# Optimization experiments

Measured on AMD Instinct MI355X. Metric: run time of the kernel, lower is better.

## Reference

```python
import jax, jax.numpy as jnp
import numpy as np

N_TOKENS = 32768
LATENT_DIM = 512
N_EMBED = 8192
BETA_COMMIT = 0.25


def setup_inputs() -> dict:
    key = jax.random.key(0)
    k_x, k_w, _ = jax.random.split(key, 3)
    x = jax.random.normal(k_x, (N_TOKENS, LATENT_DIM), dtype=jnp.float32)
    # nn.init.uniform_ -> U[0, 1)
    W = jax.random.uniform(k_w, (N_EMBED, LATENT_DIM), dtype=jnp.float32)
    temperature = jnp.ones((1,), dtype=jnp.float32)
    return {"x": x, "temperature": temperature, "W": W}


def reference(x, temperature, W):
    # out_proj is Identity (sim_vq=False, codebook_normalization=False)
    codebook = W  # [K, D]
    # Squared-Euclidean pairwise distances: [N, K]
    dist = (
        jnp.sum(x * x, axis=1, keepdims=True)
        + jnp.sum(codebook * codebook, axis=1)[None, :]
        - 2.0 * (x @ codebook.T)
    )
    ids = jnp.argmin(dist, axis=1)  # [N]
    emb = codebook[ids]             # gather nearest code, [N, D]
    # Straight-through estimator (training STE path)
    emb_out = x + jax.lax.stop_gradient(emb - x)
    # QuantizeLoss(beta): codebook loss + beta * commitment loss
    codebook_loss = jnp.mean(jnp.sum((jax.lax.stop_gradient(x) - emb) ** 2, axis=-1))
    commit_loss = jnp.mean(jnp.sum((x - jax.lax.stop_gradient(emb)) ** 2, axis=-1))
    loss = codebook_loss + BETA_COMMIT * commit_loss
    return emb_out, ids, loss
```

## Files before the change

kernel.cpp:

```cpp
#include <hip/hip_runtime.h>
#include <math.h>

#define NTOK 32768
#define DIM 512
#define KC 8192

#define BM 256
#define BN 256
#define HSTEPS 16
#define VSTEPS 48
#define NBUF 4
#define STEP_U16 8192

typedef unsigned short u16;
typedef _Float16 half8 __attribute__((ext_vector_type(8)));
typedef float f32x4 __attribute__((ext_vector_type(4)));

__device__ __forceinline__ void gload16(const void* g, void* l) {
    __builtin_amdgcn_global_load_lds(
        (const __attribute__((address_space(1))) unsigned int*)(void*)g,
        (__attribute__((address_space(3))) unsigned int*)l, 16, 0, 0);
}

__global__ __launch_bounds__(256) void c2_kernel(const float* __restrict__ W,
                                                 float* __restrict__ c2) {
    int wid = threadIdx.x >> 6;
    int lane = threadIdx.x & 63;
    int row = blockIdx.x * 4 + wid;
    const float* wr = W + (size_t)row * DIM;
    float s = 0.f;
#pragma unroll
    for (int q = 0; q < 2; ++q) {
        float4 v = *(const float4*)(wr + q * 256 + lane * 4);
        s += v.x * v.x + v.y * v.y + v.z * v.z + v.w * v.w;
    }
#pragma unroll
    for (int off = 32; off > 0; off >>= 1) s += __shfl_down(s, off);
    if (lane == 0) c2[row] = s;
}

__global__ __launch_bounds__(256) void loss_kernel(const float* __restrict__ partials,
                                                   float* __restrict__ lossp) {
    __shared__ float red[256];
    float s = 0.f;
    for (int idx = threadIdx.x; idx < NTOK / 4; idx += 256) s += partials[idx];
    red[threadIdx.x] = s;
    __syncthreads();
    for (int off = 128; off > 0; off >>= 1) {
        if (threadIdx.x < off) red[threadIdx.x] += red[threadIdx.x + off];
        __syncthreads();
    }
    if (threadIdx.x == 0) lossp[0] = 1.25f * red[0] / (float)NTOK;
}

__global__ void init_keys_kernel(unsigned long long* keys) {
    keys[blockIdx.x * 256 + threadIdx.x] = ~0ull;
}

__global__ __launch_bounds__(256) void split_kernel(const float* __restrict__ src,
                                                    u16* __restrict__ dst) {
    int lane = threadIdx.x & 63;
    int wid = threadIdx.x >> 6;
    int row = blockIdx.x * 64 + lane;
    int s = blockIdx.y * 4 + wid;
    const float* p = src + (size_t)row * DIM + s * 32;
    int tile = row >> 8, Rl = row & 255, swz = (Rl >> 1) & 3;
    u16* baseH = dst + ((size_t)(tile * 32 + s) * 256 + Rl) * 32;
    u16* baseL = baseH + (size_t)HSTEPS * STEP_U16;
#pragma unroll
    for (int c = 0; c < 4; ++c) {
        float4 va = ((const float4*)p)[c * 2];
        float4 vb = ((const float4*)p)[c * 2 + 1];
        float f[8] = {va.x, va.y, va.z, va.w, vb.x, vb.y, vb.z, vb.w};
        unsigned H[4], L[4];
#pragma unroll
        for (int j = 0; j < 4; ++j) {
            _Float16 h0 = (_Float16)f[2 * j];
            _Float16 g0 = (_Float16)(f[2 * j] - (float)h0);
            _Float16 h1 = (_Float16)f[2 * j + 1];
            _Float16 g1 = (_Float16)(f[2 * j + 1] - (float)h1);
            H[j] = (unsigned)__builtin_bit_cast(u16, h0) |
                   ((unsigned)__builtin_bit_cast(u16, h1) << 16);
            L[j] = (unsigned)__builtin_bit_cast(u16, g0) |
                   ((unsigned)__builtin_bit_cast(u16, g1) << 16);
        }
        int slot = (c ^ swz) * 8;
        *(uint4*)(baseH + slot) = uint4{H[0], H[1], H[2], H[3]};
        *(uint4*)(baseL + slot) = uint4{L[0], L[1], L[2], L[3]};
    }
}

__global__ __launch_bounds__(512, 2) void argmin_mfma_kernel(
    const u16* __restrict__ xscr, const u16* __restrict__ wscr,
    const float* __restrict__ c2, unsigned long long* __restrict__ keys) {
    __shared__ __align__(16) u16 Ab[NBUF][STEP_U16];
    __shared__ __align__(16) u16 Bb[NBUF][STEP_U16];

    int cpx = (int)gridDim.x >> 3;
    int bid = (int)blockIdx.x;
    int wg = (bid & 7) * cpx + (bid >> 3);
    int tcol = wg & 31;
    int trow = wg >> 5;

    const int tid = threadIdx.x;
    const int lane = tid & 63;
    const int w = tid >> 6;
    const int wr = w >> 2;
    const int wc = w & 3;

    const u16* gA = xscr + (size_t)trow * (32 * STEP_U16);
    const u16* gB = wscr + (size_t)tcol * (32 * STEP_U16);

    const int l15 = lane & 15, q = lane >> 4;
    float c2v[4];
    const int colbase = tcol * 256 + wc * 64 + l15;
#pragma unroll
    for (int n = 0; n < 4; ++n) c2v[n] = c2[colbase + n * 16];

    f32x4 acc[8][4];
#pragma unroll
    for (int m = 0; m < 8; ++m)
#pragma unroll
        for (int n = 0; n < 4; ++n) acc[m][n] = f32x4{0.f, 0.f, 0.f, 0.f};

    const int swz = (l15 >> 1) & 3;
    const int aoff0 = (wr * 128 + l15) * 32 + (q ^ swz) * 8;
    const int boff0 = (wc * 64 + l15) * 32 + (q ^ swz) * 8;
    const int wo = w * 512;
    const int lo8 = lane * 8;

#pragma unroll
    for (int p = 0; p < 3; ++p) {
        const u16* ga = gA + (size_t)p * STEP_U16;
        const u16* gb = gB + (size_t)p * STEP_U16;
#pragma unroll
        for (int r = 0; r < 2; ++r) {
            gload16(ga + r * 4096 + wo + lo8, Ab[p] + r * 4096 + wo);
            gload16(gb + r * 4096 + wo + lo8, Bb[p] + r * 4096 + wo);
        }
    }
    asm volatile("s_waitcnt vmcnt(8)" ::: "memory");
    __builtin_amdgcn_s_barrier();
    __builtin_amdgcn_sched_barrier(0);

#pragma unroll 4
    for (int v = 0; v < VSTEPS; ++v) {
        if (v + 3 < VSTEPS) {
            int u = v + 3;
            int sa = (u < 32) ? u : u - 32;
            int sb = (u < 16) ? u : u - 16;
            const u16* ga = gA + (size_t)sa * STEP_U16;
            const u16* gb = gB + (size_t)sb * STEP_U16;
            u16* la = Ab[u & 3];
            u16* lb = Bb[u & 3];
#pragma unroll
            for (int r = 0; r < 2; ++r) {
                gload16(ga + r * 4096 + wo + lo8, la + r * 4096 + wo);
                gload16(gb + r * 4096 + wo + lo8, lb + r * 4096 + wo);
            }
        }
        const u16* A = Ab[v & 3];
        const u16* B = Bb[v & 3];
        half8 b[4], a[8];
#pragma unroll
        for (int n = 0; n < 4; ++n) b[n] = *(const half8*)(B + boff0 + n * 512);
#pragma unroll
        for (int m = 0; m < 8; ++m) a[m] = *(const half8*)(A + aoff0 + m * 512);
        __builtin_amdgcn_s_setprio(1);
#pragma unroll
        for (int m = 0; m < 8; ++m)
#pragma unroll
            for (int n = 0; n < 4; ++n)
                acc[m][n] = __builtin_amdgcn_mfma_f32_16x16x32_f16(a[m], b[n], acc[m][n], 0, 0, 0);
        __builtin_amdgcn_s_setprio(0);
        asm volatile("s_waitcnt vmcnt(8)" ::: "memory");
        __builtin_amdgcn_s_barrier();
        __builtin_amdgcn_sched_barrier(0);
    }

    unsigned long long* kbuf = (unsigned long long*)&Ab[0][0];
#pragma unroll
    for (int m = 0; m < 8; ++m) {
#pragma unroll
        for (int r = 0; r < 4; ++r) {
            float bv = 3.4e38f;
            int bi = 0;
#pragma unroll
            for (int n = 0; n < 4; ++n) {
                float sc = c2v[n] - 2.0f * acc[m][n][r];
                int idx = colbase + n * 16;
                if (sc < bv) { bv = sc; bi = idx; }
            }
#pragma unroll
            for (int off = 1; off < 16; off <<= 1) {
                float ov = __shfl_xor(bv, off);
                int oi = __shfl_xor(bi, off);
                if (ov < bv || (ov == bv && oi < bi)) { bv = ov; bi = oi; }
            }
            if (l15 == 0) {
                unsigned u = __float_as_uint(bv);
                u = (u & 0x80000000u) ? ~u : (u | 0x80000000u);
                kbuf[wc * 256 + wr * 128 + m * 16 + q * 4 + r] =
                    ((unsigned long long)u << 32) | (unsigned)bi;
            }
        }
    }
    __syncthreads();
    if (tid < 256) {
        unsigned long long k = kbuf[tid];
#pragma unroll
        for (int c = 1; c < 4; ++c) {
            unsigned long long o = kbuf[c * 256 + tid];
            if (o < k) k = o;
        }
        atomicMin(&keys[trow * 256 + tid], k);
    }
}

__global__ __launch_bounds__(256) void gather_keys_kernel(
    const float* __restrict__ x, const float* __restrict__ W,
    const unsigned long long* __restrict__ keys, float* __restrict__ emb_out,
    float* __restrict__ idsf, float* __restrict__ partials) {
    int wid = threadIdx.x >> 6;
    int lane = threadIdx.x & 63;
    int tok = blockIdx.x * 4 + wid;
    int id = (int)(unsigned)(keys[tok] & 0xffffffffull);
    if (lane == 0) idsf[tok] = (float)id;
    const float* wr = W + (size_t)id * DIM;
    const float* xr = x + (size_t)tok * DIM;
    float* orow = emb_out + (size_t)tok * DIM;
    float s = 0.f;
#pragma unroll
    for (int q = 0; q < 2; ++q) {
        int d = q * 256 + lane * 4;
        float4 wv = *(const float4*)(wr + d);
        float4 xv = *(const float4*)(xr + d);
        float4 e = {xv.x + (wv.x - xv.x), xv.y + (wv.y - xv.y),
                    xv.z + (wv.z - xv.z), xv.w + (wv.w - xv.w)};
        *(float4*)(orow + d) = e;
        float dx = xv.x - wv.x, dy = xv.y - wv.y, dz = xv.z - wv.z, dw = xv.w - wv.w;
        s += dx * dx + dy * dy + dz * dz + dw * dw;
    }
#pragma unroll
    for (int off = 32; off > 0; off >>= 1) s += __shfl_down(s, off);
    __shared__ float bsum[4];
    if (lane == 0) bsum[wid] = s;
    __syncthreads();
    if (threadIdx.x == 0)
        partials[blockIdx.x] = bsum[0] + bsum[1] + bsum[2] + bsum[3];
}

#define FBN 64
#define FBK 64
#define FDC 32
#define FPAD 68
__global__ __launch_bounds__(256) void argmin_kernel(const float* __restrict__ x,
                                                     const float* __restrict__ W,
                                                     const float* __restrict__ c2,
                                                     float* __restrict__ idsf) {
    __shared__ float xs[FDC][FPAD];
    __shared__ float wt[FDC][FPAD];
    __shared__ float c2s[FBK];
    __shared__ float redv[16][FBN];
    __shared__ int redi[16][FBN];
    const int tid = threadIdx.x;
    const int n0 = blockIdx.x * FBN;
    const int i = tid & 15;
    const int j = tid >> 4;
    float bestv[4];
    int besti[4];
#pragma unroll
    for (int t = 0; t < 4; ++t) { bestv[t] = 3.4e38f; besti[t] = 0; }
    for (int k0 = 0; k0 < KC; k0 += FBK) {
        __syncthreads();
        if (tid < FBK) c2s[tid] = c2[k0 + tid];
        float acc[4][4];
#pragma unroll
        for (int a = 0; a < 4; ++a)
#pragma unroll
            for (int b = 0; b < 4; ++b) acc[a][b] = 0.f;
        for (int d0 = 0; d0 < DIM; d0 += FDC) {
            __syncthreads();
#pragma unroll
            for (int r = 0; r < 2; ++r) {
                int f = tid + r * 256;
                int tok = f >> 3;
                int dq = f & 7;
                float4 xv = *(const float4*)(x + (size_t)(n0 + tok) * DIM + d0 + dq * 4);
                float4 wv = *(const float4*)(W + (size_t)(k0 + tok) * DIM + d0 + dq * 4);
                xs[dq * 4 + 0][tok] = xv.x; xs[dq * 4 + 1][tok] = xv.y;
                xs[dq * 4 + 2][tok] = xv.z; xs[dq * 4 + 3][tok] = xv.w;
                wt[dq * 4 + 0][tok] = wv.x; wt[dq * 4 + 1][tok] = wv.y;
                wt[dq * 4 + 2][tok] = wv.z; wt[dq * 4 + 3][tok] = wv.w;
            }
            __syncthreads();
#pragma unroll
            for (int d = 0; d < FDC; ++d) {
                float4 xv = *(const float4*)(&xs[d][i * 4]);
                float4 wv = *(const float4*)(&wt[d][j * 4]);
#pragma unroll
                for (int a = 0; a < 4; ++a) {
                    float xa = (a == 0) ? xv.x : (a == 1) ? xv.y : (a == 2) ? xv.z : xv.w;
                    acc[a][0] = fmaf(xa, wv.x, acc[a][0]);
                    acc[a][1] = fmaf(xa, wv.y, acc[a][1]);
                    acc[a][2] = fmaf(xa, wv.z, acc[a][2]);
                    acc[a][3] = fmaf(xa, wv.w, acc[a][3]);
                }
            }
        }
#pragma unroll
        for (int ti = 0; ti < 4; ++ti)
#pragma unroll
            for (int cj = 0; cj < 4; ++cj) {
                float s = c2s[j * 4 + cj] - 2.f * acc[ti][cj];
                int kk = k0 + j * 4 + cj;
                if (s < bestv[ti]) { bestv[ti] = s; besti[ti] = kk; }
            }
    }
#pragma unroll
    for (int ti = 0; ti < 4; ++ti) {
        redv[j][i * 4 + ti] = bestv[ti];
        redi[j][i * 4 + ti] = besti[ti];
    }
    __syncthreads();
    if (tid < FBN) {
        float bv = redv[0][tid];
        int bi = redi[0][tid];
#pragma unroll
        for (int jj = 1; jj < 16; ++jj) {
            float v = redv[jj][tid];
            int ii = redi[jj][tid];
            if (v < bv || (v == bv && ii < bi)) { bv = v; bi = ii; }
        }
        idsf[n0 + tid] = (float)bi;
    }
}

__global__ __launch_bounds__(256) void gather_kernel(const float* __restrict__ x,
                                                     const float* __restrict__ W,
                                                     const float* __restrict__ idsf,
                                                     float* __restrict__ emb_out,
                                                     float* __restrict__ partials) {
    int wid = threadIdx.x >> 6;
    int lane = threadIdx.x & 63;
    int tok = blockIdx.x * 4 + wid;
    int id = (int)idsf[tok];
    const float* wr = W + (size_t)id * DIM;
    const float* xr = x + (size_t)tok * DIM;
    float* orow = emb_out + (size_t)tok * DIM;
    float s = 0.f;
#pragma unroll
    for (int q = 0; q < 2; ++q) {
        int d = q * 256 + lane * 4;
        float4 wv = *(const float4*)(wr + d);
        float4 xv = *(const float4*)(xr + d);
        float4 e = {xv.x + (wv.x - xv.x), xv.y + (wv.y - xv.y),
                    xv.z + (wv.z - xv.z), xv.w + (wv.w - xv.w)};
        *(float4*)(orow + d) = e;
        float dx = xv.x - wv.x, dy = xv.y - wv.y, dz = xv.z - wv.z, dw = xv.w - wv.w;
        s += dx * dx + dy * dy + dz * dz + dw * dw;
    }
#pragma unroll
    for (int off = 32; off > 0; off >>= 1) s += __shfl_down(s, off);
    __shared__ float bsum[4];
    if (lane == 0) bsum[wid] = s;
    __syncthreads();
    if (threadIdx.x == 0)
        partials[blockIdx.x] = bsum[0] + bsum[1] + bsum[2] + bsum[3];
}

extern "C" void kernel_launch(void* const* d_in, const int* in_sizes, int n_in,
                              void* d_out, int out_size, void* d_ws, size_t ws_size,
                              hipStream_t stream) {
    const float* x = (const float*)d_in[0];
    const float* W = (const float*)d_in[2];

    float* out = (float*)d_out;
    float* emb_out = out;
    float* idsf = out + (size_t)NTOK * DIM;
    float* lossp = idsf + NTOK;

    const size_t W12_BYTES = (size_t)KC * DIM * 4;
    const size_t KEYS_BYTES = (size_t)NTOK * 8;
    size_t need = W12_BYTES + KEYS_BYTES + (size_t)KC * 4 + (size_t)(NTOK / 4) * 4;

    if (ws_size >= need) {
        u16* w12 = (u16*)d_ws;
        unsigned long long* keys = (unsigned long long*)((char*)d_ws + W12_BYTES);
        float* c2 = (float*)((char*)keys + KEYS_BYTES);
        float* partials = c2 + KC;
        u16* x12 = (u16*)emb_out;

        split_kernel<<<dim3(NTOK / 64, 4), 256, 0, stream>>>(x, x12);
        split_kernel<<<dim3(KC / 64, 4), 256, 0, stream>>>(W, w12);
        c2_kernel<<<KC / 4, 256, 0, stream>>>(W, c2);
        init_keys_kernel<<<NTOK / 256, 256, 0, stream>>>(keys);
        argmin_mfma_kernel<<<(NTOK / BM) * (KC / BN), 512, 0, stream>>>(x12, w12, c2, keys);
        gather_keys_kernel<<<NTOK / 4, 256, 0, stream>>>(x, W, keys, emb_out, idsf, partials);
        loss_kernel<<<1, 256, 0, stream>>>(partials, lossp);
    } else {
        float* c2 = (float*)d_ws;
        float* partials = c2 + KC;
        c2_kernel<<<KC / 4, 256, 0, stream>>>(W, c2);
        argmin_kernel<<<NTOK / FBN, 256, 0, stream>>>(x, W, c2, idsf);
        gather_kernel<<<NTOK / 4, 256, 0, stream>>>(x, W, idsf, emb_out, partials);
        loss_kernel<<<1, 256, 0, stream>>>(partials, lossp);
    }
}
```

Before: 958.7 us.

## Split GEMM main loop into two half-phases interleaving LDS reads, prefetch and MFMA

```diff
diff --git a/kernel.cpp b/kernel.cpp
--- a/kernel.cpp
+++ b/kernel.cpp
@@ -133,11 +133,10 @@
     for (int p = 0; p < 3; ++p) {
         const u16* ga = gA + (size_t)p * STEP_U16;
         const u16* gb = gB + (size_t)p * STEP_U16;
-#pragma unroll
-        for (int r = 0; r < 2; ++r) {
-            gload16(ga + r * 4096 + wo + lo8, Ab[p] + r * 4096 + wo);
-            gload16(gb + r * 4096 + wo + lo8, Bb[p] + r * 4096 + wo);
-        }
+        gload16(ga + wo + lo8, Ab[p] + wo);
+        gload16(ga + 4096 + wo + lo8, Ab[p] + 4096 + wo);
+        gload16(gb + wo + lo8, Bb[p] + wo);
+        gload16(gb + 4096 + wo + lo8, Bb[p] + 4096 + wo);
     }
     asm volatile("s_waitcnt vmcnt(8)" ::: "memory");
     __builtin_amdgcn_s_barrier();
@@ -145,37 +144,69 @@
 
 #pragma unroll 4
     for (int v = 0; v < VSTEPS; ++v) {
-        if (v + 3 < VSTEPS) {
+        const u16* A = Ab[v & 3];
+        const u16* B = Bb[v & 3];
+        const bool pf = (v + 3 < VSTEPS);
+        const u16* ga = nullptr; const u16* gb = nullptr;
+        u16* la = nullptr; u16* lb = nullptr;
+        if (pf) {
             int u = v + 3;
             int sa = (u < 32) ? u : u - 32;
             int sb = (u < 16) ? u : u - 16;
-            const u16* ga = gA + (size_t)sa * STEP_U16;
-            const u16* gb = gB + (size_t)sb * STEP_U16;
-            u16* la = Ab[u & 3];
-            u16* lb = Bb[u & 3];
-#pragma unroll
-            for (int r = 0; r < 2; ++r) {
-                gload16(ga + r * 4096 + wo + lo8, la + r * 4096 + wo);
-                gload16(gb + r * 4096 + wo + lo8, lb + r * 4096 + wo);
-            }
-        }
-        const u16* A = Ab[v & 3];
-        const u16* B = Bb[v & 3];
-        half8 b[4], a[8];
-#pragma unroll
-        for (int n = 0; n < 4; ++n) b[n] = *(const half8*)(B + boff0 + n * 512);
-#pragma unroll
-        for (int m = 0; m < 8; ++m) a[m] = *(const half8*)(A + aoff0 + m * 512);
+            ga = gA + (size_t)sa * STEP_U16;
+            gb = gB + (size_t)sb * STEP_U16;
+            la = Ab[u & 3];
+            lb = Bb[u & 3];
+        }
+
+        half8 b_[4], a0_[4];
+#pragma unroll
+        for (int n = 0; n < 4; ++n) b_[n] = *(const half8*)(B + boff0 + n * 512);
+#pragma unroll
+        for (int m = 0; m < 4; ++m) a0_[m] = *(const half8*)(A + aoff0 + m * 512);
+        if (pf) {
+            gload16(ga + wo + lo8, la + wo);
+            gload16(ga + 4096 + wo + lo8, la + 4096 + wo);
+        }
+        __builtin_amdgcn_s_barrier();
+        asm volatile("s_waitcnt lgkmcnt(0)" ::: "memory");
+        __builtin_amdgcn_sched_barrier(0);
         __builtin_amdgcn_s_setprio(1);
 #pragma unroll
-        for (int m = 0; m < 8; ++m)
+        for (int m = 0; m < 4; ++m)
 #pragma unroll
             for (int n = 0; n < 4; ++n)
-                acc[m][n] = __builtin_amdgcn_mfma_f32_16x16x32_f16(a[m], b[n], acc[m][n], 0, 0, 0);
+                acc[m][n] = __builtin_amdgcn_mfma_f32_16x16x32_f16(a0_[m], b_[n], acc[m][n], 0, 0, 0);
         __builtin_amdgcn_s_setprio(0);
-        asm volatile("s_waitcnt vmcnt(8)" ::: "memory");
+        __builtin_amdgcn_sched_barrier(0);
         __builtin_amdgcn_s_barrier();
+
+        half8 a1_[4];
+#pragma unroll
+        for (int m = 0; m < 4; ++m) a1_[m] = *(const half8*)(A + aoff0 + (m + 4) * 512);
+        if (pf) {
+            gload16(gb + wo + lo8, lb + wo);
+            gload16(gb + 4096 + wo + lo8, lb + 4096 + wo);
+        }
+        __builtin_amdgcn_s_barrier();
+        asm volatile("s_waitcnt lgkmcnt(0)" ::: "memory");
         __builtin_amdgcn_sched_barrier(0);
+        __builtin_amdgcn_s_setprio(1);
+#pragma unroll
+        for (int m = 0; m < 4; ++m)
+#pragma unroll
+            for (int n = 0; n < 4; ++n)
+                acc[m + 4][n] = __builtin_amdgcn_mfma_f32_16x16x32_f16(a1_[m], b_[n], acc[m + 4][n], 0, 0, 0);
+        __builtin_amdgcn_s_setprio(0);
+        __builtin_amdgcn_sched_barrier(0);
+        if (v < VSTEPS - 3) {
+            asm volatile("s_waitcnt vmcnt(8)" ::: "memory");
+        } else if (v == VSTEPS - 3) {
+            asm volatile("s_waitcnt vmcnt(4)" ::: "memory");
+        } else if (v == VSTEPS - 2) {
+            asm volatile("s_waitcnt vmcnt(0)" ::: "memory");
+        }
+        __builtin_amdgcn_s_barrier();
     }
 
     unsigned long long* kbuf = (unsigned long long*)&Ab[0][0];
```

Result: slower. 1.021 ms (+6.5%).

## Restructure split-fp16 GEMM loop to load hi/lo tiles once per K-step

Applied to the files above, without the earlier changes.

```diff
diff --git a/kernel.cpp b/kernel.cpp
--- a/kernel.cpp
+++ b/kernel.cpp
@@ -8,8 +8,6 @@
 #define BM 256
 #define BN 256
 #define HSTEPS 16
-#define VSTEPS 48
-#define NBUF 4
 #define STEP_U16 8192
 
 typedef unsigned short u16;
@@ -93,8 +91,10 @@
 __global__ __launch_bounds__(512, 2) void argmin_mfma_kernel(
     const u16* __restrict__ xscr, const u16* __restrict__ wscr,
     const float* __restrict__ c2, unsigned long long* __restrict__ keys) {
-    __shared__ __align__(16) u16 Ab[NBUF][STEP_U16];
-    __shared__ __align__(16) u16 Bb[NBUF][STEP_U16];
+    __shared__ __align__(16) u16 AH[2][STEP_U16];
+    __shared__ __align__(16) u16 AL[2][STEP_U16];
+    __shared__ __align__(16) u16 BH[2][STEP_U16];
+    __shared__ __align__(16) u16 BL[2][STEP_U16];
 
     int cpx = (int)gridDim.x >> 3;
     int bid = (int)blockIdx.x;
@@ -126,59 +126,75 @@
     const int swz = (l15 >> 1) & 3;
     const int aoff0 = (wr * 128 + l15) * 32 + (q ^ swz) * 8;
     const int boff0 = (wc * 64 + l15) * 32 + (q ^ swz) * 8;
-    const int wo = w * 512;
+    const int wo = w * 1024;
     const int lo8 = lane * 8;
 
-#pragma unroll
-    for (int p = 0; p < 3; ++p) {
-        const u16* ga = gA + (size_t)p * STEP_U16;
-        const u16* gb = gB + (size_t)p * STEP_U16;
-#pragma unroll
-        for (int r = 0; r < 2; ++r) {
-            gload16(ga + r * 4096 + wo + lo8, Ab[p] + r * 4096 + wo);
-            gload16(gb + r * 4096 + wo + lo8, Bb[p] + r * 4096 + wo);
-        }
-    }
-    asm volatile("s_waitcnt vmcnt(8)" ::: "memory");
-    __builtin_amdgcn_s_barrier();
-    __builtin_amdgcn_sched_barrier(0);
-
-#pragma unroll 4
-    for (int v = 0; v < VSTEPS; ++v) {
-        if (v + 3 < VSTEPS) {
-            int u = v + 3;
-            int sa = (u < 32) ? u : u - 32;
-            int sb = (u < 16) ? u : u - 16;
-            const u16* ga = gA + (size_t)sa * STEP_U16;
-            const u16* gb = gB + (size_t)sb * STEP_U16;
-            u16* la = Ab[u & 3];
-            u16* lb = Bb[u & 3];
-#pragma unroll
-            for (int r = 0; r < 2; ++r) {
-                gload16(ga + r * 4096 + wo + lo8, la + r * 4096 + wo);
-                gload16(gb + r * 4096 + wo + lo8, lb + r * 4096 + wo);
-            }
-        }
-        const u16* A = Ab[v & 3];
-        const u16* B = Bb[v & 3];
-        half8 b[4], a[8];
-#pragma unroll
-        for (int n = 0; n < 4; ++n) b[n] = *(const half8*)(B + boff0 + n * 512);
-#pragma unroll
-        for (int m = 0; m < 8; ++m) a[m] = *(const half8*)(A + aoff0 + m * 512);
-        __builtin_amdgcn_s_setprio(1);
-#pragma unroll
-        for (int m = 0; m < 8; ++m)
-#pragma unroll
-            for (int n = 0; n < 4; ++n)
-                acc[m][n] = __builtin_amdgcn_mfma_f32_16x16x32_f16(a[m], b[n], acc[m][n], 0, 0, 0);
-        __builtin_amdgcn_s_setprio(0);
-        asm volatile("s_waitcnt vmcnt(8)" ::: "memory");
+    {
+        const u16* ah = gA;                       const u16* al = gA + 16 * STEP_U16;
+        const u16* bh = gB;                       const u16* bl = gB + 16 * STEP_U16;
+        gload16(ah + wo + lo8, AH[0] + wo);       gload16(ah + wo + 512 + lo8, AH[0] + wo + 512);
+        gload16(al + wo + lo8, AL[0] + wo);       gload16(al + wo + 512 + lo8, AL[0] + wo + 512);
+        gload16(bh + wo + lo8, BH[0] + wo);       gload16(bh + wo + 512 + lo8, BH[0] + wo + 512);
+        gload16(bl + wo + lo8, BL[0] + wo);       gload16(bl + wo + 512 + lo8, BL[0] + wo + 512);
+    }
+
+#pragma unroll 2
+    for (int c = 0; c < HSTEPS; ++c) {
+        const int b = c & 1;
+        asm volatile("s_waitcnt vmcnt(0)" ::: "memory");
         __builtin_amdgcn_s_barrier();
         __builtin_amdgcn_sched_barrier(0);
-    }
-
-    unsigned long long* kbuf = (unsigned long long*)&Ab[0][0];
+
+        if (c + 1 < HSTEPS) {
+            const u16* ah = gA + (size_t)(c + 1) * STEP_U16;
+            const u16* al = ah + 16 * STEP_U16;
+            const u16* bh = gB + (size_t)(c + 1) * STEP_U16;
+            const u16* bl = bh + 16 * STEP_U16;
+            u16* dah = AH[b ^ 1]; u16* dal = AL[b ^ 1];
+            u16* dbh = BH[b ^ 1]; u16* dbl = BL[b ^ 1];
+            gload16(ah + wo + lo8, dah + wo);     gload16(ah + wo + 512 + lo8, dah + wo + 512);
+            gload16(al + wo + lo8, dal + wo);     gload16(al + wo + 512 + lo8, dal + wo + 512);
+            gload16(bh + wo + lo8, dbh + wo);     gload16(bh + wo + 512 + lo8, dbh + wo + 512);
+            gload16(bl + wo + lo8, dbl + wo);     gload16(bl + wo + 512 + lo8, dbl + wo + 512);
+        }
+
+        half8 bhv[4], ahv[8];
+#pragma unroll
+        for (int n = 0; n < 4; ++n) bhv[n] = *(const half8*)(BH[b] + boff0 + n * 512);
+#pragma unroll
+        for (int m = 0; m < 8; ++m) ahv[m] = *(const half8*)(AH[b] + aoff0 + m * 512);
+        __builtin_amdgcn_s_setprio(1);
+#pragma unroll
+        for (int m = 0; m < 8; ++m)
+#pragma unroll
+            for (int n = 0; n < 4; ++n)
+                acc[m][n] = __builtin_amdgcn_mfma_f32_16x16x32_f16(ahv[m], bhv[n], acc[m][n], 0, 0, 0);
+        __builtin_amdgcn_s_setprio(0);
+
+        half8 alv[8];
+#pragma unroll
+        for (int m = 0; m < 8; ++m) alv[m] = *(const half8*)(AL[b] + aoff0 + m * 512);
+        __builtin_amdgcn_s_setprio(1);
+#pragma unroll
+        for (int m = 0; m < 8; ++m)
+#pragma unroll
+            for (int n = 0; n < 4; ++n)
+                acc[m][n] = __builtin_amdgcn_mfma_f32_16x16x32_f16(alv[m], bhv[n], acc[m][n], 0, 0, 0);
+        __builtin_amdgcn_s_setprio(0);
+
+        half8 blv[4];
+#pragma unroll
+        for (int n = 0; n < 4; ++n) blv[n] = *(const half8*)(BL[b] + boff0 + n * 512);
+        __builtin_amdgcn_s_setprio(1);
+#pragma unroll
+        for (int m = 0; m < 8; ++m)
+#pragma unroll
+            for (int n = 0; n < 4; ++n)
+                acc[m][n] = __builtin_amdgcn_mfma_f32_16x16x32_f16(ahv[m], blv[n], acc[m][n], 0, 0, 0);
+        __builtin_amdgcn_s_setprio(0);
+    }
+
+    unsigned long long* kbuf = (unsigned long long*)&AH[0][0];
 #pragma unroll
     for (int m = 0; m < 8; ++m) {
 #pragma unroll
```

Result: no change. 971.0 us (+1.3%).
